# Performance work log

Measured on AMD Instinct MI355X. Metric: run time of the kernel, lower is better.

## Reference

```python
import jax, jax.numpy as jnp
import numpy as np

BLOCK = 16
NUM_HEADS = 12
EMBED = 768
LN_EPS = 1e-6


def setup_inputs() -> dict:
    key = jax.random.key(0)
    ks = jax.random.split(key, 6)
    H = W = 1024
    x = jax.random.normal(ks[0], (H, W), dtype=jnp.float32)
    # Conv2d(1, EMBED, kernel=BLOCK, stride=BLOCK) weights, flattened to [E, b*b]
    proj_w = jax.random.normal(ks[1], (EMBED, BLOCK * BLOCK), dtype=jnp.float32) * 0.02
    proj_b = jax.random.normal(ks[2], (EMBED,), dtype=jnp.float32) * 0.02
    ln_g = jnp.ones((EMBED,), dtype=jnp.float32)
    ln_b = jnp.zeros((EMBED,), dtype=jnp.float32)
    # nn.Linear(E, 3E, bias=False): weight [3E, E]
    qkv_w = jax.random.normal(ks[3], (3 * EMBED, EMBED), dtype=jnp.float32) * 0.02
    return {"x": x, "proj_w": proj_w, "proj_b": proj_b,
            "ln_g": ln_g, "ln_b": ln_b, "qkv_w": qkv_w}


def reference(x, proj_w, proj_b, ln_g, ln_b, qkv_w):
    H, W = x.shape
    b = BLOCK
    # Patch embed: conv with kernel=stride=b on a single-channel image is
    # exactly patchify + matmul. Token order matches flatten(2) (row-major).
    patches = x.reshape(H // b, b, W // b, b).transpose(0, 2, 1, 3)
    patches = patches.reshape((H // b) * (W // b), b * b)      # [N, b*b]
    tok = patches @ proj_w.T + proj_b                          # [N, E]

    # LayerNorm (eps=1e-6)
    mu = jnp.mean(tok, axis=-1, keepdims=True)
    var = jnp.mean(jnp.square(tok - mu), axis=-1, keepdims=True)
    tok = (tok - mu) * jax.lax.rsqrt(var + LN_EPS) * ln_g + ln_b

    # Attention (batch = 1)
    N, C = tok.shape
    h, d = NUM_HEADS, C // NUM_HEADS
    qkv = (tok @ qkv_w.T).reshape(N, 3, h, d)                  # [N, 3, h, d]
    q = qkv[:, 0].transpose(1, 0, 2)                            # [h, N, d]
    k = qkv[:, 1].transpose(1, 0, 2)
    v = qkv[:, 2].transpose(1, 0, 2)
    scale = d ** -0.5
    attn = jax.nn.softmax(jnp.einsum('hnd,hmd->hnm', q, k) * scale, axis=-1)
    out = jnp.einsum('hnm,hmd->hnd', attn, v)                   # [h, N, d]
    out = out.transpose(1, 0, 2).reshape(N, C)                  # [N, C]
    return out[None]                                            # [1, N, C]
```

## Files before the change

### kernel.cpp

```cpp
#include <hip/hip_runtime.h>
#include <hip/hip_bf16.h>

typedef __bf16 bf16_t;
typedef __attribute__((ext_vector_type(8))) __bf16 bf16x8;
typedef __attribute__((ext_vector_type(4))) __bf16 bf16x4;
typedef __attribute__((ext_vector_type(4))) float f32x4;
typedef __attribute__((ext_vector_type(4))) unsigned int uint4v;

#define QSCALE 0.1803368801111204f

static __device__ inline void glds16(const bf16_t* g, bf16_t* l) {
    __builtin_amdgcn_global_load_lds(
        (__attribute__((address_space(1))) const void*)g,
        (__attribute__((address_space(3))) void*)l,
        16, 0, 0);
}

static __device__ inline float hwexp2(float x) {
#if __has_builtin(__builtin_amdgcn_exp2f)
    return __builtin_amdgcn_exp2f(x);
#else
    float r;
    asm("v_exp_f32 %0, %1" : "=v"(r) : "v"(x));
    return r;
#endif
}

static __device__ inline unsigned int pack_trunc(float lo, float hi) {
    return __builtin_amdgcn_perm(__builtin_bit_cast(unsigned int, hi),
                                 __builtin_bit_cast(unsigned int, lo),
                                 0x07060302u);
}

__global__ void cvt_kernel(const float* __restrict__ in, bf16_t* __restrict__ out, int n4) {
    int i = blockIdx.x * 256 + threadIdx.x;
    if (i < n4) {
        float4 v = ((const float4*)in)[i];
        bf16x4 o = {(bf16_t)v.x, (bf16_t)v.y, (bf16_t)v.z, (bf16_t)v.w};
        ((bf16x4*)out)[i] = o;
    }
}

__global__ __launch_bounds__(256) void patch_gemm(const float* __restrict__ x,
                                                  const float* __restrict__ pw,
                                                  const float* __restrict__ pb,
                                                  float* __restrict__ tok) {
    const int bn = blockIdx.x;
    const int bm = blockIdx.y;
    const int tid = threadIdx.x;

    __shared__ bf16_t At[64][264];
    __shared__ bf16_t Bt[64][264];

    #pragma unroll
    for (int t = 0; t < 16; t++) {
        int linear = tid + t * 256;
        int ml = linear >> 6;
        int kv = (linear & 63) << 2;
        int n = bm * 64 + ml;
        int pr = n >> 6, pc = n & 63;
        int i = kv >> 4, j = kv & 15;
        float4 v = *(const float4*)(x + (pr * 16 + i) * 1024 + pc * 16 + j);
        bf16x4 o = {(bf16_t)v.x, (bf16_t)v.y, (bf16_t)v.z, (bf16_t)v.w};
        *(bf16x4*)(&At[ml][kv]) = o;
    }
    #pragma unroll
    for (int t = 0; t < 8; t++) {
        int linear = tid + t * 256;
        int nl = linear >> 5;
        int kv = (linear & 31) << 3;
        const float* src = pw + (size_t)(bn * 64 + nl) * 256 + kv;
        float4 v0 = *(const float4*)(src);
        float4 v1 = *(const float4*)(src + 4);
        bf16x8 o = {(bf16_t)v0.x, (bf16_t)v0.y, (bf16_t)v0.z, (bf16_t)v0.w,
                    (bf16_t)v1.x, (bf16_t)v1.y, (bf16_t)v1.z, (bf16_t)v1.w};
        *(bf16x8*)(&Bt[nl][kv]) = o;
    }
    __syncthreads();

    const int lane = tid & 63, wid = tid >> 6, ln = lane & 15, quad = lane >> 4;
    f32x4 acc[4];
    #pragma unroll
    for (int s = 0; s < 4; s++) acc[s] = {0.f, 0.f, 0.f, 0.f};

    #pragma unroll
    for (int kk = 0; kk < 8; kk++) {
        bf16x8 af = *(const bf16x8*)(&At[wid * 16 + ln][kk * 32 + quad * 8]);
        #pragma unroll
        for (int s = 0; s < 4; s++) {
            bf16x8 bfr = *(const bf16x8*)(&Bt[s * 16 + ln][kk * 32 + quad * 8]);
            acc[s] = __builtin_amdgcn_mfma_f32_16x16x32_bf16(af, bfr, acc[s], 0, 0, 0);
        }
    }

    #pragma unroll
    for (int s = 0; s < 4; s++) {
        int e = bn * 64 + s * 16 + ln;
        float bias = pb[e];
        #pragma unroll
        for (int r = 0; r < 4; r++) {
            int m = bm * 64 + wid * 16 + quad * 4 + r;
            tok[(size_t)m * 768 + e] = acc[s][r] + bias;
        }
    }
}

__global__ __launch_bounds__(256) void ln_kernel(const float* __restrict__ tok,
                                                 const float* __restrict__ g,
                                                 const float* __restrict__ b,
                                                 bf16_t* __restrict__ out) {
    const int n = blockIdx.x;
    const int tid = threadIdx.x;
    const float* row = tok + (size_t)n * 768;
    float x0 = row[tid], x1 = row[tid + 256], x2 = row[tid + 512];
    float s = x0 + x1 + x2;
    float s2 = x0 * x0 + x1 * x1 + x2 * x2;
    #pragma unroll
    for (int off = 32; off; off >>= 1) {
        s += __shfl_xor(s, off);
        s2 += __shfl_xor(s2, off);
    }
    __shared__ float ws1[4], ws2[4];
    int wid = tid >> 6;
    if ((tid & 63) == 0) { ws1[wid] = s; ws2[wid] = s2; }
    __syncthreads();
    s = ws1[0] + ws1[1] + ws1[2] + ws1[3];
    s2 = ws2[0] + ws2[1] + ws2[2] + ws2[3];
    float mu = s * (1.f / 768.f);
    float var = s2 * (1.f / 768.f) - mu * mu;
    float r = rsqrtf(var + 1e-6f);
    bf16_t* orow = out + (size_t)n * 768;
    orow[tid]       = (bf16_t)((x0 - mu) * r * g[tid]       + b[tid]);
    orow[tid + 256] = (bf16_t)((x1 - mu) * r * g[tid + 256] + b[tid + 256]);
    orow[tid + 512] = (bf16_t)((x2 - mu) * r * g[tid + 512] + b[tid + 512]);
}

__global__ __launch_bounds__(256) void qkv_gemm(const bf16_t* __restrict__ tokb,
                                                const bf16_t* __restrict__ wq,
                                                bf16_t* __restrict__ qb,
                                                bf16_t* __restrict__ kswz,
                                                bf16_t* __restrict__ vswz) {
    const int bn = blockIdx.x;
    const int bm = blockIdx.y;
    const int tid = threadIdx.x;
    const int wid = tid >> 6, lane = tid & 63;
    const int ln = lane & 15, quad = lane >> 4;
    const int wm = wid & 1, wn = wid >> 1;

    __shared__ bf16_t Asw[2][8192];
    __shared__ bf16_t Bsw[2][4096];

    f32x4 acc[4][2];
    #pragma unroll
    for (int sm = 0; sm < 4; sm++)
        #pragma unroll
        for (int sn = 0; sn < 2; sn++) acc[sm][sn] = {0.f, 0.f, 0.f, 0.f};

    auto stage = [&](int kb0, int buf) {
        #pragma unroll
        for (int i = 0; i < 4; i++) {
            int L = wid * 256 + i * 64 + lane;
            int r = L >> 3, c = L & 7;
            int gc = c ^ (r & 7);
            glds16(tokb + (size_t)(bm * 128 + r) * 768 + kb0 + gc * 8,
                   Asw[buf] + (wid * 256 + i * 64) * 8);
        }
        #pragma unroll
        for (int i = 0; i < 2; i++) {
            int L = wid * 128 + i * 64 + lane;
            int r = L >> 3, c = L & 7;
            int gc = c ^ (r & 7);
            glds16(wq + (size_t)(bn * 64 + r) * 768 + kb0 + gc * 8,
                   Bsw[buf] + (wid * 128 + i * 64) * 8);
        }
    };

    auto compute = [&](const bf16_t* Ab, const bf16_t* Bb) {
        #pragma unroll
        for (int kk = 0; kk < 2; kk++) {
            const int c = (kk * 4 + quad) ^ (ln & 7);
            bf16x8 af[4], bfr[2];
            #pragma unroll
            for (int sm = 0; sm < 4; sm++) {
                int row = wm * 64 + sm * 16 + ln;
                af[sm] = *(const bf16x8*)(Ab + (row * 8 + c) * 8);
            }
            #pragma unroll
            for (int sn = 0; sn < 2; sn++) {
                int row = wn * 32 + sn * 16 + ln;
                bfr[sn] = *(const bf16x8*)(Bb + (row * 8 + c) * 8);
            }
            #pragma unroll
            for (int sm = 0; sm < 4; sm++)
                #pragma unroll
                for (int sn = 0; sn < 2; sn++)
                    acc[sm][sn] = __builtin_amdgcn_mfma_f32_16x16x32_bf16(af[sm], bfr[sn], acc[sm][sn], 0, 0, 0);
        }
    };

    stage(0, 0);

    for (int s = 0; s < 12; s += 2) {
        __builtin_amdgcn_s_barrier();
        stage((s + 1) * 64, 1);
        __builtin_amdgcn_s_waitcnt(0x0F76);
        __builtin_amdgcn_s_barrier();
        compute(Asw[0], Bsw[0]);
        __builtin_amdgcn_s_barrier();
        if (s + 2 < 12) {
            stage((s + 2) * 64, 0);
            __builtin_amdgcn_s_waitcnt(0x0F76);
        } else {
            __builtin_amdgcn_s_waitcnt(0x0F70);
        }
        __builtin_amdgcn_s_barrier();
        compute(Asw[1], Bsw[1]);
    }

    const int sidx = bn / 12;
    const int head = bn % 12;
    #pragma unroll
    for (int sn = 0; sn < 2; sn++) {
        int dc = wn * 32 + sn * 16 + ln;
        #pragma unroll
        for (int sm = 0; sm < 4; sm++) {
            #pragma unroll
            for (int r = 0; r < 4; r++) {
                int m = bm * 128 + wm * 64 + sm * 16 + quad * 4 + r;
                float v = acc[sm][sn][r];
                if (sidx == 0) {
                    qb[((size_t)(head * 4096 + m)) * 64 + dc] = (bf16_t)(v * QSCALE);
                } else if (sidx == 1) {
                    bf16_t val = (bf16_t)v;
                    int kt = m >> 6, sb = (m >> 4) & 3, lnk = m & 15;
                    int half = dc >> 5, quadk = (dc >> 3) & 3, j = dc & 7;
                    int l = quadk * 16 + lnk;
                    kswz[((size_t)(head * 64 + kt)) * 4096 + sb * 1024 + half * 512 + l * 8 + j] = val;
                } else {
                    bf16_t val = (bf16_t)v;
                    int kt = m >> 6, keyl = m & 63;
                    int sblk = keyl >> 4;
                    int mm = sblk >> 1, tb = sblk & 1;
                    int w16 = keyl & 15, qv = w16 >> 2, jj = w16 & 3;
                    int jp = tb * 4 + jj;
                    int db = dc >> 4, lnv = dc & 15;
                    int l = qv * 16 + lnv;
                    vswz[((size_t)(head * 64 + kt)) * 4096 + ((mm * 4 + db) * 64 + l) * 8 + jp] = val;
                }
            }
        }
    }
}

__global__ __launch_bounds__(128, 2) void attn_partial(const bf16_t* __restrict__ qbuf,
                                                       const bf16_t* __restrict__ kswz,
                                                       const bf16_t* __restrict__ vswz,
                                                       float* __restrict__ raw0,
                                                       float* __restrict__ raw1,
                                                       float* __restrict__ l_part) {
    const int h = blockIdx.y;
    const int chunk = blockIdx.z;
    const int tid = threadIdx.x;
    const int wid = tid >> 6;
    const int lane = tid & 63;
    const int ln = lane & 15, quad = lane >> 4;
    const int q0 = blockIdx.x * 128;

    __shared__ bf16_t Kf[2][4096];
    __shared__ bf16_t Vf[2][4096];

    bf16x8 qf[4][2];
    #pragma unroll
    for (int g = 0; g < 4; g++) {
        const int q0g = q0 + wid * 64 + g * 16;
        const bf16_t* qrow = qbuf + ((size_t)h * 4096 + q0g + ln) * 64;
        qf[g][0] = *(const bf16x8*)(qrow + quad * 8);
        qf[g][1] = *(const bf16x8*)(qrow + 32 + quad * 8);
    }

    bf16x8 ones;
    #pragma unroll
    for (int i = 0; i < 8; i++) ones[i] = (bf16_t)1.0f;

    const bf16_t* kg = kswz + (size_t)h * 64 * 4096 + (size_t)chunk * 32 * 4096;
    const bf16_t* vg = vswz + (size_t)h * 64 * 4096 + (size_t)chunk * 32 * 4096;

    f32x4 accO[4][4];
    f32x4 accL[4];
    #pragma unroll
    for (int g = 0; g < 4; g++) {
        accL[g] = {0.f, 0.f, 0.f, 0.f};
        #pragma unroll
        for (int d = 0; d < 4; d++) accO[g][d] = {0.f, 0.f, 0.f, 0.f};
    }

    auto stage = [&](int tile, int buf) {
        const bf16_t* kt_g = kg + (size_t)tile * 4096;
        const bf16_t* vt_g = vg + (size_t)tile * 4096;
        #pragma unroll
        for (int i = 0; i < 4; i++) {
            glds16(kt_g + wid * 2048 + i * 512 + lane * 8, &Kf[buf][wid * 2048 + i * 512]);
            glds16(vt_g + wid * 2048 + i * 512 + lane * 8, &Vf[buf][wid * 2048 + i * 512]);
        }
    };

    auto compute = [&](const bf16_t* Kb, const bf16_t* Vb) {
        #pragma unroll
        for (int m = 0; m < 2; m++) {
            bf16x8 vf[4];
            #pragma unroll
            for (int db = 0; db < 4; db++)
                vf[db] = *(const bf16x8*)(Vb + m * 2048 + db * 512 + lane * 8);
            bf16x8 kfa0 = *(const bf16x8*)(Kb + (2 * m) * 1024 + lane * 8);
            bf16x8 kfa1 = *(const bf16x8*)(Kb + (2 * m) * 1024 + 512 + lane * 8);
            bf16x8 kfb0 = *(const bf16x8*)(Kb + (2 * m + 1) * 1024 + lane * 8);
            bf16x8 kfb1 = *(const bf16x8*)(Kb + (2 * m + 1) * 1024 + 512 + lane * 8);
            #pragma unroll
            for (int g = 0; g < 4; g++) {
                f32x4 z = {0.f, 0.f, 0.f, 0.f};
                f32x4 SA = __builtin_amdgcn_mfma_f32_16x16x32_bf16(kfa0, qf[g][0], z, 0, 0, 0);
                SA = __builtin_amdgcn_mfma_f32_16x16x32_bf16(kfa1, qf[g][1], SA, 0, 0, 0);
                f32x4 SB = __builtin_amdgcn_mfma_f32_16x16x32_bf16(kfb0, qf[g][0], z, 0, 0, 0);
                SB = __builtin_amdgcn_mfma_f32_16x16x32_bf16(kfb1, qf[g][1], SB, 0, 0, 0);

                float e0 = hwexp2(SA[0]), e1 = hwexp2(SA[1]), e2 = hwexp2(SA[2]), e3 = hwexp2(SA[3]);
                float e4 = hwexp2(SB[0]), e5 = hwexp2(SB[1]), e6 = hwexp2(SB[2]), e7 = hwexp2(SB[3]);
                uint4v u = {pack_trunc(e0, e1), pack_trunc(e2, e3),
                            pack_trunc(e4, e5), pack_trunc(e6, e7)};
                bf16x8 pb = __builtin_bit_cast(bf16x8, u);
                accL[g] = __builtin_amdgcn_mfma_f32_16x16x32_bf16(ones, pb, accL[g], 0, 0, 0);
                #pragma unroll
                for (int db = 0; db < 4; db++)
                    accO[g][db] = __builtin_amdgcn_mfma_f32_16x16x32_bf16(vf[db], pb, accO[g][db], 0, 0, 0);
            }
        }
    };

    stage(0, 0);

    for (int kt = 0; kt < 32; kt += 2) {
        __builtin_amdgcn_s_barrier();
        stage(kt + 1, 1);
        __builtin_amdgcn_s_waitcnt(0x0F78);
        __builtin_amdgcn_s_barrier();
        compute(&Kf[0][0], &Vf[0][0]);
        __builtin_amdgcn_s_barrier();
        if (kt + 2 < 32) {
            stage(kt + 2, 0);
            __builtin_amdgcn_s_waitcnt(0x0F78);
        } else {
            __builtin_amdgcn_s_waitcnt(0x0F70);
        }
        __builtin_amdgcn_s_barrier();
        compute(&Kf[1][0], &Vf[1][0]);
    }

    float* base = chunk ? raw1 : raw0;
    #pragma unroll
    for (int g = 0; g < 4; g++) {
        const int qg = q0 + wid * 64 + g * 16 + ln;
        if (quad == 0) l_part[(size_t)chunk * 49152 + h * 4096 + qg] = accL[g][0];
        float* op = base + (size_t)qg * 768 + h * 64 + quad * 4;
        #pragma unroll
        for (int db = 0; db < 4; db++)
            *(f32x4*)(op + db * 16) = accO[g][db];
    }
}

__global__ __launch_bounds__(256) void norm_kernel(const float* __restrict__ raw0,
                                                   const float* __restrict__ raw1,
                                                   const float* __restrict__ l_part,
                                                   float* __restrict__ out) {
    const int q = blockIdx.x;
    const int tid = threadIdx.x;
    __shared__ float linv[12];
    if (tid < 12)
        linv[tid] = 1.0f / (l_part[tid * 4096 + q] + l_part[49152 + tid * 4096 + q]);
    __syncthreads();
    #pragma unroll
    for (int t = 0; t < 3; t++) {
        int c = tid + t * 256;
        size_t idx = (size_t)q * 768 + c;
        out[idx] = (raw0[idx] + raw1[idx]) * linv[c >> 6];
    }
}

extern "C" void kernel_launch(void* const* d_in, const int* in_sizes, int n_in,
                              void* d_out, int out_size, void* d_ws, size_t ws_size,
                              hipStream_t stream) {
    const float* x      = (const float*)d_in[0];
    const float* proj_w = (const float*)d_in[1];
    const float* proj_b = (const float*)d_in[2];
    const float* ln_g   = (const float*)d_in[3];
    const float* ln_b   = (const float*)d_in[4];
    const float* qkv_w  = (const float*)d_in[5];
    float* out = (float*)d_out;

    char* ws = (char*)d_ws;
    float*  tok_pre = (float*)(ws + 0);
    bf16_t* tok_b   = (bf16_t*)(ws + 12582912);
    bf16_t* pw_b    = (bf16_t*)(ws + 18874368);
    bf16_t* qw_b    = (bf16_t*)(ws + 19267584);
    bf16_t* qbuf    = (bf16_t*)(ws + 22806528);
    bf16_t* kswz    = (bf16_t*)(ws + 29097984);
    bf16_t* vswz    = (bf16_t*)(ws + 35389440);
    float*  raw0    = tok_pre;
    float*  raw1    = out;
    float*  l_part  = (float*)pw_b;

    cvt_kernel<<<1728, 256, 0, stream>>>(qkv_w, qw_b, 442368);
    patch_gemm<<<dim3(12, 64), 256, 0, stream>>>(x, proj_w, proj_b, tok_pre);
    ln_kernel<<<4096, 256, 0, stream>>>(tok_pre, ln_g, ln_b, tok_b);
    qkv_gemm<<<dim3(36, 32), 256, 0, stream>>>(tok_b, qw_b, qbuf, kswz, vswz);
    attn_partial<<<dim3(32, 12, 2), 128, 0, stream>>>(qbuf, kswz, vswz, raw0, raw1, l_part);
    norm_kernel<<<4096, 256, 0, stream>>>(raw0, raw1, l_part, out);
}
```

Before: 185.6 us.

## Split attention KV range across two wave pairs per block with LDS reduction

```diff
diff --git a/kernel.cpp b/kernel.cpp
--- a/kernel.cpp
+++ b/kernel.cpp
@@ -252,7 +252,7 @@
     }
 }
 
-__global__ __launch_bounds__(128, 2) void attn_partial(const bf16_t* __restrict__ qbuf,
+__global__ __launch_bounds__(256, 2) void attn_partial(const bf16_t* __restrict__ qbuf,
                                                        const bf16_t* __restrict__ kswz,
                                                        const bf16_t* __restrict__ vswz,
                                                        float* __restrict__ raw0,
@@ -264,15 +264,16 @@
     const int wid = tid >> 6;
     const int lane = tid & 63;
     const int ln = lane & 15, quad = lane >> 4;
+    const int qh = wid & 1;
+    const int kh = wid >> 1;
     const int q0 = blockIdx.x * 128;
 
-    __shared__ bf16_t Kf[2][4096];
-    __shared__ bf16_t Vf[2][4096];
+    __shared__ bf16_t SMEM[2][2][2][4096];
 
     bf16x8 qf[4][2];
     #pragma unroll
     for (int g = 0; g < 4; g++) {
-        const int q0g = q0 + wid * 64 + g * 16;
+        const int q0g = q0 + qh * 64 + g * 16;
         const bf16_t* qrow = qbuf + ((size_t)h * 4096 + q0g + ln) * 64;
         qf[g][0] = *(const bf16x8*)(qrow + quad * 8);
         qf[g][1] = *(const bf16x8*)(qrow + 32 + quad * 8);
@@ -282,8 +283,8 @@
     #pragma unroll
     for (int i = 0; i < 8; i++) ones[i] = (bf16_t)1.0f;
 
-    const bf16_t* kg = kswz + (size_t)h * 64 * 4096 + (size_t)chunk * 32 * 4096;
-    const bf16_t* vg = vswz + (size_t)h * 64 * 4096 + (size_t)chunk * 32 * 4096;
+    const bf16_t* kg = kswz + (size_t)h * 64 * 4096 + (size_t)(chunk * 32 + kh * 16) * 4096;
+    const bf16_t* vg = vswz + (size_t)h * 64 * 4096 + (size_t)(chunk * 32 + kh * 16) * 4096;
 
     f32x4 accO[4][4];
     f32x4 accL[4];
@@ -297,10 +298,12 @@
     auto stage = [&](int tile, int buf) {
         const bf16_t* kt_g = kg + (size_t)tile * 4096;
         const bf16_t* vt_g = vg + (size_t)tile * 4096;
+        bf16_t* kl = &SMEM[0][kh][buf][qh * 2048];
+        bf16_t* vl = &SMEM[1][kh][buf][qh * 2048];
         #pragma unroll
         for (int i = 0; i < 4; i++) {
-            glds16(kt_g + wid * 2048 + i * 512 + lane * 8, &Kf[buf][wid * 2048 + i * 512]);
-            glds16(vt_g + wid * 2048 + i * 512 + lane * 8, &Vf[buf][wid * 2048 + i * 512]);
+            glds16(kt_g + qh * 2048 + i * 512 + lane * 8, kl + i * 512);
+            glds16(vt_g + qh * 2048 + i * 512 + lane * 8, vl + i * 512);
         }
     };
 
@@ -338,32 +341,52 @@
 
     stage(0, 0);
 
-    for (int kt = 0; kt < 32; kt += 2) {
+    for (int kt = 0; kt < 16; kt += 2) {
         __builtin_amdgcn_s_barrier();
         stage(kt + 1, 1);
         __builtin_amdgcn_s_waitcnt(0x0F78);
         __builtin_amdgcn_s_barrier();
-        compute(&Kf[0][0], &Vf[0][0]);
-        __builtin_amdgcn_s_barrier();
-        if (kt + 2 < 32) {
+        compute(&SMEM[0][kh][0][0], &SMEM[1][kh][0][0]);
+        __builtin_amdgcn_s_barrier();
+        if (kt + 2 < 16) {
             stage(kt + 2, 0);
             __builtin_amdgcn_s_waitcnt(0x0F78);
         } else {
             __builtin_amdgcn_s_waitcnt(0x0F70);
         }
         __builtin_amdgcn_s_barrier();
-        compute(&Kf[1][0], &Vf[1][0]);
-    }
-
-    float* base = chunk ? raw1 : raw0;
-    #pragma unroll
-    for (int g = 0; g < 4; g++) {
-        const int qg = q0 + wid * 64 + g * 16 + ln;
-        if (quad == 0) l_part[(size_t)chunk * 49152 + h * 4096 + qg] = accL[g][0];
-        float* op = base + (size_t)qg * 768 + h * 64 + quad * 4;
-        #pragma unroll
-        for (int db = 0; db < 4; db++)
-            *(f32x4*)(op + db * 16) = accO[g][db];
+        compute(&SMEM[0][kh][1][0], &SMEM[1][kh][1][0]);
+    }
+
+    __syncthreads();
+    float* comb  = (float*)&SMEM[0][0][0][0];
+    float* combl = (float*)((char*)&SMEM[0][0][0][0] + 36864);
+    if (kh == 1) {
+        #pragma unroll
+        for (int g = 0; g < 4; g++) {
+            const int lq = qh * 64 + g * 16 + ln;
+            #pragma unroll
+            for (int db = 0; db < 4; db++)
+                *(f32x4*)&comb[lq * 68 + db * 16 + quad * 4] = accO[g][db];
+            if (quad == 0) combl[lq] = accL[g][0];
+        }
+    }
+    __syncthreads();
+    if (kh == 0) {
+        float* base = chunk ? raw1 : raw0;
+        #pragma unroll
+        for (int g = 0; g < 4; g++) {
+            const int lq = qh * 64 + g * 16 + ln;
+            const int qg = q0 + lq;
+            float lsum = accL[g][0] + combl[lq];
+            if (quad == 0) l_part[(size_t)chunk * 49152 + h * 4096 + qg] = lsum;
+            float* op = base + (size_t)qg * 768 + h * 64 + quad * 4;
+            #pragma unroll
+            for (int db = 0; db < 4; db++) {
+                f32x4 o = accO[g][db] + *(const f32x4*)&comb[lq * 68 + db * 16 + quad * 4];
+                *(f32x4*)(op + db * 16) = o;
+            }
+        }
     }
 }
 
@@ -412,6 +435,6 @@
     patch_gemm<<<dim3(12, 64), 256, 0, stream>>>(x, proj_w, proj_b, tok_pre);
     ln_kernel<<<4096, 256, 0, stream>>>(tok_pre, ln_g, ln_b, tok_b);
     qkv_gemm<<<dim3(36, 32), 256, 0, stream>>>(tok_b, qw_b, qbuf, kswz, vswz);
-    attn_partial<<<dim3(32, 12, 2), 128, 0, stream>>>(qbuf, kswz, vswz, raw0, raw1, l_part);
+    attn_partial<<<dim3(32, 12, 2), 256, 0, stream>>>(qbuf, kswz, vswz, raw0, raw1, l_part);
     norm_kernel<<<4096, 256, 0, stream>>>(raw0, raw1, l_part, out);
 }
```

Result: faster. 176.2 us (-5.1%).
